# Performance work log

Hardware: AMD Instinct MI355X
Metric: run time of the kernel (lower is better)

Reference implementation:

```python
import jax, jax.numpy as jnp
import numpy as np

N_NODES = 50000


def setup_inputs() -> dict:
    key = jax.random.key(0)
    k1, k2, k3, k4 = jax.random.split(key, 4)
    in_c, hid = 256, 128
    x = jax.random.normal(k1, (N_NODES, in_c), dtype=jnp.float32)
    edge_index = jax.random.randint(k2, (2, 800000), 0, N_NODES, dtype=jnp.int32)
    # GCNConv weight (glorot) and bias
    W_conv = jax.random.normal(k3, (in_c, hid), dtype=jnp.float32) * (1.0 / np.sqrt(in_c))
    b_conv = jnp.zeros((hid,), dtype=jnp.float32)
    # Final Linear (xavier_uniform per reset_parameters)
    limit = np.sqrt(6.0 / (hid + in_c))
    W_lin = jax.random.uniform(k4, (hid, in_c), dtype=jnp.float32, minval=-limit, maxval=limit)
    b_lin = jnp.zeros((in_c,), dtype=jnp.float32)
    return {"x": x, "edge_index": edge_index, "W_conv": W_conv, "b_conv": b_conv,
            "W_lin": W_lin, "b_lin": b_lin}


def _gcn_conv(x, edge_index, W, b):
    n = x.shape[0]
    # add self-loops (standard GCN normalization)
    loop = jnp.arange(n, dtype=edge_index.dtype)
    src = jnp.concatenate([edge_index[0], loop])
    dst = jnp.concatenate([edge_index[1], loop])
    # transform first (in_c -> hid) so the edge gather moves the smaller dim
    h = x @ W  # [N, hid]
    deg = jax.ops.segment_sum(jnp.ones_like(dst, dtype=h.dtype), dst, num_segments=n)
    dinv = jnp.where(deg > 0, jax.lax.rsqrt(deg), 0.0)
    norm = dinv[src] * dinv[dst]  # [E+N]
    msg = h[src] * norm[:, None]  # [E+N, hid]
    out = jax.ops.segment_sum(msg, dst, num_segments=n)
    return out + b


def reference(x, edge_index, W_conv, b_conv, W_lin, b_lin):
    h = _gcn_conv(x, edge_index, W_conv, b_conv)  # [N, hid]
    # dropout p=0.0 -> identity
    return h @ W_lin + b_lin  # [N, in_c]
```

## Files before the change

### kernel.cpp

```cpp
#include <hip/hip_runtime.h>


#define N_NODES 50000
#define N_EDGES 800000
#define IN_C 256
#define HID 128
#define SCAN_BLOCKS ((N_NODES + 255) / 256)
#define GEMM_MBLK ((N_NODES + 63) / 64)

#define OFF_H    0UL
#define OFF_CONV 12800000UL
#define OFF_DEG  25600000UL
#define OFF_CNT  25800000UL
#define OFF_RP   26000000UL
#define OFF_DINV 26200064UL
#define OFF_CSR  26400064UL
#define OFF_BSUM 29600064UL
#define OFF_WT1  29601088UL
#define OFF_WT2  29666624UL

typedef __attribute__((ext_vector_type(8))) short bf16x8;
typedef __attribute__((ext_vector_type(4))) float f32x4;

__device__ __forceinline__ ushort f2bf(float x) {
    unsigned u = __float_as_uint(x);
    u += 0x7fffu + ((u >> 16) & 1u);
    return (ushort)(u >> 16);
}

__global__ void deg_kernel(const int* __restrict__ dst, int* __restrict__ deg, int e) {
    int i = blockIdx.x * blockDim.x + threadIdx.x;
    if (i < e) atomicAdd(&deg[dst[i]], 1);
}

__global__ __launch_bounds__(256) void scan_blocks_kernel(
    const int* __restrict__ deg, int* __restrict__ row_ptr,
    int* __restrict__ bsums, int n)
{
    __shared__ int tmp[256];
    int tid = threadIdx.x;
    int i = blockIdx.x * 256 + tid;
    int v = (i < n) ? deg[i] : 0;
    int orig = v;
    tmp[tid] = v;
    __syncthreads();
    #pragma unroll
    for (int off = 1; off < 256; off <<= 1) {
        int t = (tid >= off) ? tmp[tid - off] : 0;
        __syncthreads();
        tmp[tid] += t;
        __syncthreads();
    }
    if (i < n) row_ptr[i] = tmp[tid] - orig;
    if (tid == 255) bsums[blockIdx.x] = tmp[255];
}

__global__ __launch_bounds__(256) void scan_sums_kernel(int* __restrict__ bsums, int nb) {
    __shared__ int tmp[256];
    int tid = threadIdx.x;
    int v = (tid < nb) ? bsums[tid] : 0;
    int orig = v;
    tmp[tid] = v;
    __syncthreads();
    #pragma unroll
    for (int off = 1; off < 256; off <<= 1) {
        int t = (tid >= off) ? tmp[tid - off] : 0;
        __syncthreads();
        tmp[tid] += t;
        __syncthreads();
    }
    if (tid < nb) bsums[tid] = tmp[tid] - orig;
}

__global__ __launch_bounds__(256) void finalize_kernel(
    const int* __restrict__ deg, int* __restrict__ row_ptr,
    const int* __restrict__ bsums, float* __restrict__ dinv, int n)
{
    int i = blockIdx.x * 256 + threadIdx.x;
    if (i < n) {
        row_ptr[i] += bsums[blockIdx.x];
        dinv[i] = rsqrtf((float)(deg[i] + 1));
    }
    if (i == 0) row_ptr[n] = N_EDGES;
}

__global__ void bucket_kernel(const int* __restrict__ src, const int* __restrict__ dst,
                              const int* __restrict__ row_ptr, int* __restrict__ cnt,
                              int* __restrict__ csr_src, int e) {
    int i = blockIdx.x * blockDim.x + threadIdx.x;
    if (i < e) {
        int d = dst[i];
        int slot = row_ptr[d] + atomicAdd(&cnt[d], 1);
        csr_src[slot] = src[i];
    }
}

__global__ void transpose_w_kernel(const float* __restrict__ W, ushort* __restrict__ Wt,
                                   int K, int N) {
    int i = blockIdx.x * 256 + threadIdx.x;
    if (i < N * K) {
        int n = i / K, k = i % K;
        Wt[i] = f2bf(W[k * N + n]);
    }
}

template <bool A_IS_BF16, bool BF16OUT>
__global__ __launch_bounds__(256) void mfma_gemm_kernel(
    const void* __restrict__ Av, const ushort* __restrict__ Bt,
    const float* __restrict__ bias, void* __restrict__ Cv,
    int M, int N, int K)
{
    constexpr int LDK = 40;
    __shared__ ushort As[64 * LDK];
    __shared__ ushort Bs[128 * LDK];
    int tid = threadIdx.x;
    int wave = tid >> 6, lane = tid & 63;
    int quad = lane >> 4, l16 = lane & 15;
    int wm0 = (wave >> 1) * 32, wn0 = (wave & 1) * 64;
    int bm = blockIdx.x * 64, bn = blockIdx.y * 128;

    f32x4 acc[2][4] = {};

    for (int k0 = 0; k0 < K; k0 += 32) {
        {
            int row = tid >> 2, col = (tid & 3) * 8;
            int grow = bm + row;
            if (A_IS_BF16) {
                bf16x8 v = {};
                if (grow < M)
                    v = *(const bf16x8*)((const ushort*)Av + (size_t)grow * K + k0 + col);
                *(bf16x8*)&As[row * LDK + col] = v;
            } else {
                float4 v0 = make_float4(0.f, 0.f, 0.f, 0.f);
                float4 v1 = make_float4(0.f, 0.f, 0.f, 0.f);
                if (grow < M) {
                    const float* ap = (const float*)Av + (size_t)grow * K + k0 + col;
                    v0 = *(const float4*)ap;
                    v1 = *(const float4*)(ap + 4);
                }
                ushort t[8] = {f2bf(v0.x), f2bf(v0.y), f2bf(v0.z), f2bf(v0.w),
                               f2bf(v1.x), f2bf(v1.y), f2bf(v1.z), f2bf(v1.w)};
                *(bf16x8*)&As[row * LDK + col] = *(bf16x8*)t;
            }
        }
        {
            int ch = tid * 2;
            int n = ch >> 2;
            int kk = (ch & 3) * 8;
            const ushort* bp = Bt + (size_t)(bn + n) * K + k0 + kk;
            *(bf16x8*)&Bs[n * LDK + kk]     = *(const bf16x8*)bp;
            *(bf16x8*)&Bs[n * LDK + kk + 8] = *(const bf16x8*)(bp + 8);
        }
        __syncthreads();
        bf16x8 af[2], bfr[4];
        #pragma unroll
        for (int im = 0; im < 2; ++im)
            af[im] = *(bf16x8*)&As[(wm0 + im * 16 + l16) * LDK + quad * 8];
        #pragma unroll
        for (int in = 0; in < 4; ++in)
            bfr[in] = *(bf16x8*)&Bs[(wn0 + in * 16 + l16) * LDK + quad * 8];
        #pragma unroll
        for (int im = 0; im < 2; ++im)
            #pragma unroll
            for (int in = 0; in < 4; ++in)
                acc[im][in] = __builtin_amdgcn_mfma_f32_16x16x32_bf16(
                    af[im], bfr[in], acc[im][in], 0, 0, 0);
        __syncthreads();
    }
    #pragma unroll
    for (int im = 0; im < 2; ++im) {
        #pragma unroll
        for (int in = 0; in < 4; ++in) {
            int col = bn + wn0 + in * 16 + l16;
            float bval = bias ? bias[col] : 0.f;
            #pragma unroll
            for (int r = 0; r < 4; ++r) {
                int grow = bm + wm0 + im * 16 + quad * 4 + r;
                if (grow < M) {
                    float o = acc[im][in][r] + bval;
                    if (BF16OUT)
                        ((ushort*)Cv)[(size_t)grow * N + col] = f2bf(o);
                    else
                        ((float*)Cv)[(size_t)grow * N + col] = o;
                }
            }
        }
    }
}

__global__ __launch_bounds__(256) void gather_kernel(
    const ushort* __restrict__ hb, const int* __restrict__ row_ptr,
    const int* __restrict__ csr_src, const float* __restrict__ dinv,
    const float* __restrict__ b_conv, ushort* __restrict__ convb, int n)
{
    int wave = threadIdx.x >> 6;
    int lane = threadIdx.x & 63;
    int d = blockIdx.x * 4 + wave;
    if (d >= n) return;
    int c = lane << 1;
    float di = dinv[d];
    unsigned hv = *(const unsigned*)&hb[(size_t)d * HID + c];
    float2 acc;
    acc.x = di * __uint_as_float(hv << 16);
    acc.y = di * __uint_as_float(hv & 0xffff0000u);
    int begin = row_ptr[d], end = row_ptr[d + 1];
    int e = begin;
    for (; e + 2 <= end; e += 2) {
        int s0 = csr_src[e];
        int s1 = csr_src[e + 1];
        float w0 = dinv[s0];
        float w1 = dinv[s1];
        unsigned v0 = *(const unsigned*)&hb[(size_t)s0 * HID + c];
        unsigned v1 = *(const unsigned*)&hb[(size_t)s1 * HID + c];
        acc.x += w0 * __uint_as_float(v0 << 16);
        acc.y += w0 * __uint_as_float(v0 & 0xffff0000u);
        acc.x += w1 * __uint_as_float(v1 << 16);
        acc.y += w1 * __uint_as_float(v1 & 0xffff0000u);
    }
    if (e < end) {
        int s0 = csr_src[e];
        float w0 = dinv[s0];
        unsigned v0 = *(const unsigned*)&hb[(size_t)s0 * HID + c];
        acc.x += w0 * __uint_as_float(v0 << 16);
        acc.y += w0 * __uint_as_float(v0 & 0xffff0000u);
    }
    float ox = di * acc.x + b_conv[c];
    float oy = di * acc.y + b_conv[c + 1];
    unsigned po = ((unsigned)f2bf(oy) << 16) | (unsigned)f2bf(ox);
    *(unsigned*)&convb[(size_t)d * HID + c] = po;
}

extern "C" void kernel_launch(void* const* d_in, const int* in_sizes, int n_in,
                              void* d_out, int out_size, void* d_ws, size_t ws_size,
                              hipStream_t stream) {
    const float* x      = (const float*)d_in[0];
    const int*   ei     = (const int*)d_in[1];
    const float* W_conv = (const float*)d_in[2];
    const float* b_conv = (const float*)d_in[3];
    const float* W_lin  = (const float*)d_in[4];
    const float* b_lin  = (const float*)d_in[5];
    float* out = (float*)d_out;

    char* ws = (char*)d_ws;
    ushort* hb     = (ushort*)(ws + OFF_H);
    ushort* convb  = (ushort*)(ws + OFF_CONV);
    int*   deg     = (int*)(ws + OFF_DEG);
    int*   cnt     = (int*)(ws + OFF_CNT);
    int*   row_ptr = (int*)(ws + OFF_RP);
    float* dinv    = (float*)(ws + OFF_DINV);
    int*   csr_src = (int*)(ws + OFF_CSR);
    int*   bsums   = (int*)(ws + OFF_BSUM);
    ushort* wt_conv = (ushort*)(ws + OFF_WT1);
    ushort* wt_lin  = (ushort*)(ws + OFF_WT2);

    const int* src = ei;
    const int* dst = ei + N_EDGES;

    hipMemsetAsync(deg, 0, 400000, stream);

    deg_kernel<<<(N_EDGES + 255) / 256, 256, 0, stream>>>(dst, deg, N_EDGES);
    scan_blocks_kernel<<<SCAN_BLOCKS, 256, 0, stream>>>(deg, row_ptr, bsums, N_NODES);
    scan_sums_kernel<<<1, 256, 0, stream>>>(bsums, SCAN_BLOCKS);
    finalize_kernel<<<SCAN_BLOCKS, 256, 0, stream>>>(deg, row_ptr, bsums, dinv, N_NODES);
    bucket_kernel<<<(N_EDGES + 255) / 256, 256, 0, stream>>>(src, dst, row_ptr, cnt, csr_src, N_EDGES);

    transpose_w_kernel<<<(HID * IN_C + 255) / 256, 256, 0, stream>>>(W_conv, wt_conv, IN_C, HID);
    transpose_w_kernel<<<(IN_C * HID + 255) / 256, 256, 0, stream>>>(W_lin, wt_lin, HID, IN_C);

    mfma_gemm_kernel<false, true><<<dim3(GEMM_MBLK, HID / 128), 256, 0, stream>>>(
        x, wt_conv, nullptr, hb, N_NODES, HID, IN_C);

    gather_kernel<<<(N_NODES + 3) / 4, 256, 0, stream>>>(
        hb, row_ptr, csr_src, dinv, b_conv, convb, N_NODES);

    mfma_gemm_kernel<true, false><<<dim3(GEMM_MBLK, IN_C / 128), 256, 0, stream>>>(
        convb, wt_lin, b_lin, out, N_NODES, IN_C, HID);
}
```

Measured before the change: 279.4 us.

## Store hidden features in 32-column slices and gather per slice with 16-bit indices

The first GEMM now writes the hidden features as four column slices of [N,32] bf16 instead of row-major [N,128]. The gather kernel runs over a 2D grid with one slice per grid row, so each pass touches a roughly 3.2MB working set that stays in L2. Inside a wave, four 16-lane groups each handle a different edge and are combined with cross-lane shuffles. CSR source indices are stored as ushort, which halves index traffic but only holds while the node count stays below 65536; the second GEMM reads the sliced layout. The cost is re-reading row_ptr, indices and dinv once per slice, plus shorter 64B row reads.

```diff
diff --git a/kernel.cpp b/kernel.cpp
--- a/kernel.cpp
+++ b/kernel.cpp
@@ -15,9 +15,9 @@
 #define OFF_RP   26000000UL
 #define OFF_DINV 26200064UL
 #define OFF_CSR  26400064UL
-#define OFF_BSUM 29600064UL
-#define OFF_WT1  29601088UL
-#define OFF_WT2  29666624UL
+#define OFF_BSUM 28000064UL
+#define OFF_WT1  28001088UL
+#define OFF_WT2  28066624UL
 
 typedef __attribute__((ext_vector_type(8))) short bf16x8;
 typedef __attribute__((ext_vector_type(4))) float f32x4;
@@ -86,12 +86,12 @@
 
 __global__ void bucket_kernel(const int* __restrict__ src, const int* __restrict__ dst,
                               const int* __restrict__ row_ptr, int* __restrict__ cnt,
-                              int* __restrict__ csr_src, int e) {
+                              ushort* __restrict__ csr_src, int e) {
     int i = blockIdx.x * blockDim.x + threadIdx.x;
     if (i < e) {
         int d = dst[i];
         int slot = row_ptr[d] + atomicAdd(&cnt[d], 1);
-        csr_src[slot] = src[i];
+        csr_src[slot] = (ushort)src[i];
     }
 }
 
@@ -104,7 +104,7 @@
     }
 }
 
-template <bool A_IS_BF16, bool BF16OUT>
+template <bool A_SLICED, bool OUT_SLICED>
 __global__ __launch_bounds__(256) void mfma_gemm_kernel(
     const void* __restrict__ Av, const ushort* __restrict__ Bt,
     const float* __restrict__ bias, void* __restrict__ Cv,
@@ -125,10 +125,11 @@
         {
             int row = tid >> 2, col = (tid & 3) * 8;
             int grow = bm + row;
-            if (A_IS_BF16) {
+            if (A_SLICED) {
                 bf16x8 v = {};
                 if (grow < M)
-                    v = *(const bf16x8*)((const ushort*)Av + (size_t)grow * K + k0 + col);
+                    v = *(const bf16x8*)((const ushort*)Av +
+                          ((size_t)(k0 >> 5) * M + grow) * 32 + col);
                 *(bf16x8*)&As[row * LDK + col] = v;
             } else {
                 float4 v0 = make_float4(0.f, 0.f, 0.f, 0.f);
@@ -178,8 +179,8 @@
                 int grow = bm + wm0 + im * 16 + quad * 4 + r;
                 if (grow < M) {
                     float o = acc[im][in][r] + bval;
-                    if (BF16OUT)
-                        ((ushort*)Cv)[(size_t)grow * N + col] = f2bf(o);
+                    if (OUT_SLICED)
+                        ((ushort*)Cv)[((size_t)(col >> 5) * M + grow) * 32 + (col & 31)] = f2bf(o);
                     else
                         ((float*)Cv)[(size_t)grow * N + col] = o;
                 }
@@ -190,44 +191,41 @@
 
 __global__ __launch_bounds__(256) void gather_kernel(
     const ushort* __restrict__ hb, const int* __restrict__ row_ptr,
-    const int* __restrict__ csr_src, const float* __restrict__ dinv,
+    const ushort* __restrict__ csr_src, const float* __restrict__ dinv,
     const float* __restrict__ b_conv, ushort* __restrict__ convb, int n)
 {
     int wave = threadIdx.x >> 6;
     int lane = threadIdx.x & 63;
     int d = blockIdx.x * 4 + wave;
     if (d >= n) return;
-    int c = lane << 1;
-    float di = dinv[d];
-    unsigned hv = *(const unsigned*)&hb[(size_t)d * HID + c];
-    float2 acc;
-    acc.x = di * __uint_as_float(hv << 16);
-    acc.y = di * __uint_as_float(hv & 0xffff0000u);
+    int slice = blockIdx.y;
+    int sub = lane >> 4;
+    int l16 = lane & 15;
+    const ushort* hsl = hb + (size_t)slice * N_NODES * 32;
+
+    float2 acc = make_float2(0.f, 0.f);
     int begin = row_ptr[d], end = row_ptr[d + 1];
-    int e = begin;
-    for (; e + 2 <= end; e += 2) {
-        int s0 = csr_src[e];
-        int s1 = csr_src[e + 1];
-        float w0 = dinv[s0];
-        float w1 = dinv[s1];
-        unsigned v0 = *(const unsigned*)&hb[(size_t)s0 * HID + c];
-        unsigned v1 = *(const unsigned*)&hb[(size_t)s1 * HID + c];
-        acc.x += w0 * __uint_as_float(v0 << 16);
-        acc.y += w0 * __uint_as_float(v0 & 0xffff0000u);
-        acc.x += w1 * __uint_as_float(v1 << 16);
-        acc.y += w1 * __uint_as_float(v1 & 0xffff0000u);
-    }
-    if (e < end) {
-        int s0 = csr_src[e];
-        float w0 = dinv[s0];
-        unsigned v0 = *(const unsigned*)&hb[(size_t)s0 * HID + c];
-        acc.x += w0 * __uint_as_float(v0 << 16);
-        acc.y += w0 * __uint_as_float(v0 & 0xffff0000u);
-    }
-    float ox = di * acc.x + b_conv[c];
-    float oy = di * acc.y + b_conv[c + 1];
-    unsigned po = ((unsigned)f2bf(oy) << 16) | (unsigned)f2bf(ox);
-    *(unsigned*)&convb[(size_t)d * HID + c] = po;
+    for (int e = begin + sub; e < end; e += 4) {
+        int s = csr_src[e];
+        float w = dinv[s];
+        unsigned v = *(const unsigned*)&hsl[(size_t)s * 32 + l16 * 2];
+        acc.x += w * __uint_as_float(v << 16);
+        acc.y += w * __uint_as_float(v & 0xffff0000u);
+    }
+    acc.x += __shfl_xor(acc.x, 16); acc.y += __shfl_xor(acc.y, 16);
+    acc.x += __shfl_xor(acc.x, 32); acc.y += __shfl_xor(acc.y, 32);
+
+    if (sub == 0) {
+        float di = dinv[d];
+        unsigned hv = *(const unsigned*)&hsl[(size_t)d * 32 + l16 * 2];
+        acc.x += di * __uint_as_float(hv << 16);
+        acc.y += di * __uint_as_float(hv & 0xffff0000u);
+        int c = slice * 32 + l16 * 2;
+        float ox = di * acc.x + b_conv[c];
+        float oy = di * acc.y + b_conv[c + 1];
+        unsigned po = ((unsigned)f2bf(oy) << 16) | (unsigned)f2bf(ox);
+        *(unsigned*)&convb[((size_t)slice * N_NODES + d) * 32 + l16 * 2] = po;
+    }
 }
 
 extern "C" void kernel_launch(void* const* d_in, const int* in_sizes, int n_in,
@@ -248,7 +246,7 @@
     int*   cnt     = (int*)(ws + OFF_CNT);
     int*   row_ptr = (int*)(ws + OFF_RP);
     float* dinv    = (float*)(ws + OFF_DINV);
-    int*   csr_src = (int*)(ws + OFF_CSR);
+    ushort* csr_src = (ushort*)(ws + OFF_CSR);
     int*   bsums   = (int*)(ws + OFF_BSUM);
     ushort* wt_conv = (ushort*)(ws + OFF_WT1);
     ushort* wt_lin  = (ushort*)(ws + OFF_WT2);
@@ -270,7 +268,7 @@
     mfma_gemm_kernel<false, true><<<dim3(GEMM_MBLK, HID / 128), 256, 0, stream>>>(
         x, wt_conv, nullptr, hb, N_NODES, HID, IN_C);
 
-    gather_kernel<<<(N_NODES + 3) / 4, 256, 0, stream>>>(
+    gather_kernel<<<dim3((N_NODES + 3) / 4, 4), 256, 0, stream>>>(
         hb, row_ptr, csr_src, dinv, b_conv, convb, N_NODES);
 
     mfma_gemm_kernel<true, false><<<dim3(GEMM_MBLK, IN_C / 128), 256, 0, stream>>>(
```

After: 315.0 us. +12.7%, slower.

## Pack src index and fp16 dinv into CSR records, rank edges during degree count

Applied to the files above, without the earlier changes.

The degree kernel now saves each edge's atomic rank, so the bucket pass no longer needs a second counter array or its atomics. Bucketing is split into eight destination ranges so each block's scattered writes land in a smaller region. Each CSR entry now packs a 16-bit source index with an fp16 copy of that source's dinv, which removes a random dinv lookup per edge in the gather. The gather loop is also unrolled to four edges. In exchange, every bucket block rereads the dst array once per range, the source index only fits because the node count is below 65536, and the edge weights lose precision in fp16.

```diff
diff --git a/kernel.cpp b/kernel.cpp
--- a/kernel.cpp
+++ b/kernel.cpp
@@ -1,4 +1,5 @@
 #include <hip/hip_runtime.h>
+#include <hip/hip_fp16.h>
 
 
 #define N_NODES 50000
@@ -11,13 +12,13 @@
 #define OFF_H    0UL
 #define OFF_CONV 12800000UL
 #define OFF_DEG  25600000UL
-#define OFF_CNT  25800000UL
-#define OFF_RP   26000000UL
-#define OFF_DINV 26200064UL
-#define OFF_CSR  26400064UL
-#define OFF_BSUM 29600064UL
-#define OFF_WT1  29601088UL
-#define OFF_WT2  29666624UL
+#define OFF_RP   25800000UL
+#define OFF_DINV 26000064UL
+#define OFF_RANK 26200064UL
+#define OFF_REC  27800064UL
+#define OFF_BSUM 31000064UL
+#define OFF_WT1  31001088UL
+#define OFF_WT2  31066624UL
 
 typedef __attribute__((ext_vector_type(8))) short bf16x8;
 typedef __attribute__((ext_vector_type(4))) float f32x4;
@@ -28,9 +29,10 @@
     return (ushort)(u >> 16);
 }
 
-__global__ void deg_kernel(const int* __restrict__ dst, int* __restrict__ deg, int e) {
+__global__ void deg_kernel(const int* __restrict__ dst, int* __restrict__ deg,
+                           ushort* __restrict__ rank, int e) {
     int i = blockIdx.x * blockDim.x + threadIdx.x;
-    if (i < e) atomicAdd(&deg[dst[i]], 1);
+    if (i < e) rank[i] = (ushort)atomicAdd(&deg[dst[i]], 1);
 }
 
 __global__ __launch_bounds__(256) void scan_blocks_kernel(
@@ -84,14 +86,27 @@
     if (i == 0) row_ptr[n] = N_EDGES;
 }
 
-__global__ void bucket_kernel(const int* __restrict__ src, const int* __restrict__ dst,
-                              const int* __restrict__ row_ptr, int* __restrict__ cnt,
-                              int* __restrict__ csr_src, int e) {
-    int i = blockIdx.x * blockDim.x + threadIdx.x;
-    if (i < e) {
+#define BUCKET_BLOCKS 2048
+__global__ __launch_bounds__(256) void bucket_kernel(
+    const int* __restrict__ src, const int* __restrict__ dst,
+    const ushort* __restrict__ rank, const int* __restrict__ row_ptr,
+    const float* __restrict__ dinv, unsigned* __restrict__ rec)
+{
+    int cls = blockIdx.x & 7;
+    int blk = blockIdx.x >> 3;
+    int lo = cls * (N_NODES / 8);
+    int hi = lo + (N_NODES / 8);
+    const int CHUNK = (N_EDGES + 255) / 256;
+    int e0 = blk * CHUNK;
+    int e1 = min(e0 + CHUNK, N_EDGES);
+    for (int i = e0 + threadIdx.x; i < e1; i += 256) {
         int d = dst[i];
-        int slot = row_ptr[d] + atomicAdd(&cnt[d], 1);
-        csr_src[slot] = src[i];
+        if (d >= lo && d < hi) {
+            int s = src[i];
+            unsigned r = (unsigned)(ushort)s |
+                         ((unsigned)__half_as_ushort(__float2half_rn(dinv[s])) << 16);
+            rec[row_ptr[d] + rank[i]] = r;
+        }
     }
 }
 
@@ -190,7 +205,7 @@
 
 __global__ __launch_bounds__(256) void gather_kernel(
     const ushort* __restrict__ hb, const int* __restrict__ row_ptr,
-    const int* __restrict__ csr_src, const float* __restrict__ dinv,
+    const unsigned* __restrict__ rec, const float* __restrict__ dinv,
     const float* __restrict__ b_conv, ushort* __restrict__ convb, int n)
 {
     int wave = threadIdx.x >> 6;
@@ -205,21 +220,30 @@
     acc.y = di * __uint_as_float(hv & 0xffff0000u);
     int begin = row_ptr[d], end = row_ptr[d + 1];
     int e = begin;
-    for (; e + 2 <= end; e += 2) {
-        int s0 = csr_src[e];
-        int s1 = csr_src[e + 1];
-        float w0 = dinv[s0];
-        float w1 = dinv[s1];
+    for (; e + 4 <= end; e += 4) {
+        unsigned r0 = rec[e], r1 = rec[e + 1], r2 = rec[e + 2], r3 = rec[e + 3];
+        unsigned s0 = r0 & 0xffffu, s1 = r1 & 0xffffu, s2 = r2 & 0xffffu, s3 = r3 & 0xffffu;
+        float w0 = __half2float(__ushort_as_half((ushort)(r0 >> 16)));
+        float w1 = __half2float(__ushort_as_half((ushort)(r1 >> 16)));
+        float w2 = __half2float(__ushort_as_half((ushort)(r2 >> 16)));
+        float w3 = __half2float(__ushort_as_half((ushort)(r3 >> 16)));
         unsigned v0 = *(const unsigned*)&hb[(size_t)s0 * HID + c];
         unsigned v1 = *(const unsigned*)&hb[(size_t)s1 * HID + c];
+        unsigned v2 = *(const unsigned*)&hb[(size_t)s2 * HID + c];
+        unsigned v3 = *(const unsigned*)&hb[(size_t)s3 * HID + c];
         acc.x += w0 * __uint_as_float(v0 << 16);
         acc.y += w0 * __uint_as_float(v0 & 0xffff0000u);
         acc.x += w1 * __uint_as_float(v1 << 16);
         acc.y += w1 * __uint_as_float(v1 & 0xffff0000u);
-    }
-    if (e < end) {
-        int s0 = csr_src[e];
-        float w0 = dinv[s0];
+        acc.x += w2 * __uint_as_float(v2 << 16);
+        acc.y += w2 * __uint_as_float(v2 & 0xffff0000u);
+        acc.x += w3 * __uint_as_float(v3 << 16);
+        acc.y += w3 * __uint_as_float(v3 & 0xffff0000u);
+    }
+    for (; e < end; ++e) {
+        unsigned r0 = rec[e];
+        unsigned s0 = r0 & 0xffffu;
+        float w0 = __half2float(__ushort_as_half((ushort)(r0 >> 16)));
         unsigned v0 = *(const unsigned*)&hb[(size_t)s0 * HID + c];
         acc.x += w0 * __uint_as_float(v0 << 16);
         acc.y += w0 * __uint_as_float(v0 & 0xffff0000u);
@@ -242,27 +266,27 @@
     float* out = (float*)d_out;
 
     char* ws = (char*)d_ws;
-    ushort* hb     = (ushort*)(ws + OFF_H);
-    ushort* convb  = (ushort*)(ws + OFF_CONV);
-    int*   deg     = (int*)(ws + OFF_DEG);
-    int*   cnt     = (int*)(ws + OFF_CNT);
-    int*   row_ptr = (int*)(ws + OFF_RP);
-    float* dinv    = (float*)(ws + OFF_DINV);
-    int*   csr_src = (int*)(ws + OFF_CSR);
-    int*   bsums   = (int*)(ws + OFF_BSUM);
+    ushort* hb      = (ushort*)(ws + OFF_H);
+    ushort* convb   = (ushort*)(ws + OFF_CONV);
+    int*    deg     = (int*)(ws + OFF_DEG);
+    int*    row_ptr = (int*)(ws + OFF_RP);
+    float*  dinv    = (float*)(ws + OFF_DINV);
+    ushort* rank    = (ushort*)(ws + OFF_RANK);
+    unsigned* rec   = (unsigned*)(ws + OFF_REC);
+    int*    bsums   = (int*)(ws + OFF_BSUM);
     ushort* wt_conv = (ushort*)(ws + OFF_WT1);
     ushort* wt_lin  = (ushort*)(ws + OFF_WT2);
 
     const int* src = ei;
     const int* dst = ei + N_EDGES;
 
-    hipMemsetAsync(deg, 0, 400000, stream);
-
-    deg_kernel<<<(N_EDGES + 255) / 256, 256, 0, stream>>>(dst, deg, N_EDGES);
+    hipMemsetAsync(deg, 0, 200000, stream);
+
+    deg_kernel<<<(N_EDGES + 255) / 256, 256, 0, stream>>>(dst, deg, rank, N_EDGES);
     scan_blocks_kernel<<<SCAN_BLOCKS, 256, 0, stream>>>(deg, row_ptr, bsums, N_NODES);
     scan_sums_kernel<<<1, 256, 0, stream>>>(bsums, SCAN_BLOCKS);
     finalize_kernel<<<SCAN_BLOCKS, 256, 0, stream>>>(deg, row_ptr, bsums, dinv, N_NODES);
-    bucket_kernel<<<(N_EDGES + 255) / 256, 256, 0, stream>>>(src, dst, row_ptr, cnt, csr_src, N_EDGES);
+    bucket_kernel<<<BUCKET_BLOCKS, 256, 0, stream>>>(src, dst, rank, row_ptr, dinv, rec);
 
     transpose_w_kernel<<<(HID * IN_C + 255) / 256, 256, 0, stream>>>(W_conv, wt_conv, IN_C, HID);
     transpose_w_kernel<<<(IN_C * HID + 255) / 256, 256, 0, stream>>>(W_lin, wt_lin, HID, IN_C);
@@ -271,7 +295,7 @@
         x, wt_conv, nullptr, hb, N_NODES, HID, IN_C);
 
     gather_kernel<<<(N_NODES + 3) / 4, 256, 0, stream>>>(
-        hb, row_ptr, csr_src, dinv, b_conv, convb, N_NODES);
+        hb, row_ptr, rec, dinv, b_conv, convb, N_NODES);
 
     mfma_gemm_kernel<true, false><<<dim3(GEMM_MBLK, IN_C / 128), 256, 0, stream>>>(
         convb, wt_lin, b_lin, out, N_NODES, IN_C, HID);
```

New measurement: 238.8 us. -14.5%, faster.
